# Kernel optimization log

Measured on AMD Instinct MI355X. Metric: run time of the kernel, lower is better.

Reference implementation:

```python
import jax, jax.numpy as jnp
import numpy as np

DIM = 768
NH = 12
HD = DIM // NH
HIDDEN = 4 * DIM
Z_SIZE = (8, 8)
X_SIZE = (16, 16)
SCALE = HD ** -0.5
LN_EPS = 1e-5


def _rel_index(q_size, kv_size):
    hq, wq = q_size
    hk, wk = kv_size
    cq = np.stack(np.meshgrid(np.arange(hq), np.arange(wq), indexing='ij'), -1).reshape(-1, 2)
    ck = np.stack(np.meshgrid(np.arange(hk), np.arange(wk), indexing='ij'), -1).reshape(-1, 2)
    rel = cq[:, None, :] - ck[None, :, :]  # (Lq, Lk, 2)
    rel[..., 0] += hk - 1
    rel[..., 1] += wk - 1
    return jnp.asarray(rel[..., 0] * (wq + wk - 1) + rel[..., 1])  # (Lq, Lk)

ZX_IDX = _rel_index(Z_SIZE, X_SIZE)  # (64, 256)
XZ_IDX = _rel_index(X_SIZE, Z_SIZE)  # (256, 64)


def _ln(v, g, b):
    m = jnp.mean(v, -1, keepdims=True)
    var = jnp.var(v, -1, keepdims=True)
    return (v - m) * jax.lax.rsqrt(var + LN_EPS) * g + b


def _cross_attn(q_in, kv_in, qw, qb, kvw, kvb, pw, pb, rpb, idx):
    B, Lq, D = q_in.shape
    Lk = kv_in.shape[1]
    q = (q_in @ qw.T + qb).reshape(B, Lq, NH, HD).transpose(0, 2, 1, 3)  # (B,H,Lq,hd)
    kv = (kv_in @ kvw.T + kvb).reshape(B, Lk, 2, NH, HD).transpose(2, 0, 3, 1, 4)
    k, v = kv[0], kv[1]  # (B,H,Lk,hd)
    bias = rpb[idx].transpose(2, 0, 1)  # (H,Lq,Lk)
    attn = jnp.einsum('bhqd,bhkd->bhqk', q, k) * SCALE + bias[None]
    attn = jax.nn.softmax(attn, axis=-1)
    o = jnp.einsum('bhqk,bhkd->bhqd', attn, v).transpose(0, 2, 1, 3).reshape(B, Lq, D)
    return o @ pw.T + pb


def _mlp(v, w1, b1, w2, b2):
    return jax.nn.gelu(v @ w1.T + b1, approximate=False) @ w2.T + b2


def setup_inputs() -> dict:
    key = jax.random.key(0)
    ks = jax.random.split(key, 24)
    w = lambda k, s: jax.random.normal(k, s, jnp.float32) * 0.02
    TBL = (Z_SIZE[0] + X_SIZE[0] - 1) * (Z_SIZE[1] + X_SIZE[1] - 1)  # 529
    return {
        'z': jax.random.normal(ks[0], (64, 64, DIM), jnp.float32),
        'x': jax.random.normal(ks[1], (64, 256, DIM), jnp.float32),
        'z_ln1_g': jnp.ones((DIM,), jnp.float32), 'z_ln1_b': jnp.zeros((DIM,), jnp.float32),
        'x_ln1_g': jnp.ones((DIM,), jnp.float32), 'x_ln1_b': jnp.zeros((DIM,), jnp.float32),
        'zx_qw': w(ks[2], (DIM, DIM)), 'zx_qb': jnp.zeros((DIM,), jnp.float32),
        'zx_kvw': w(ks[3], (2 * DIM, DIM)), 'zx_kvb': jnp.zeros((2 * DIM,), jnp.float32),
        'zx_pw': w(ks[4], (DIM, DIM)), 'zx_pb': jnp.zeros((DIM,), jnp.float32),
        'zx_rpb': w(ks[5], (TBL, NH)),
        'xz_qw': w(ks[6], (DIM, DIM)), 'xz_qb': jnp.zeros((DIM,), jnp.float32),
        'xz_kvw': w(ks[7], (2 * DIM, DIM)), 'xz_kvb': jnp.zeros((2 * DIM,), jnp.float32),
        'xz_pw': w(ks[8], (DIM, DIM)), 'xz_pb': jnp.zeros((DIM,), jnp.float32),
        'xz_rpb': w(ks[9], (TBL, NH)),
        'z_ln2_g': jnp.ones((DIM,), jnp.float32), 'z_ln2_b': jnp.zeros((DIM,), jnp.float32),
        'z_fc1_w': w(ks[10], (HIDDEN, DIM)), 'z_fc1_b': jnp.zeros((HIDDEN,), jnp.float32),
        'z_fc2_w': w(ks[11], (DIM, HIDDEN)), 'z_fc2_b': jnp.zeros((DIM,), jnp.float32),
        'x_ln2_g': jnp.ones((DIM,), jnp.float32), 'x_ln2_b': jnp.zeros((DIM,), jnp.float32),
        'x_fc1_w': w(ks[12], (HIDDEN, DIM)), 'x_fc1_b': jnp.zeros((HIDDEN,), jnp.float32),
        'x_fc2_w': w(ks[13], (DIM, HIDDEN)), 'x_fc2_b': jnp.zeros((DIM,), jnp.float32),
    }


def reference(z, x, z_ln1_g, z_ln1_b, x_ln1_g, x_ln1_b,
              zx_qw, zx_qb, zx_kvw, zx_kvb, zx_pw, zx_pb, zx_rpb,
              xz_qw, xz_qb, xz_kvw, xz_kvb, xz_pw, xz_pb, xz_rpb,
              z_ln2_g, z_ln2_b, z_fc1_w, z_fc1_b, z_fc2_w, z_fc2_b,
              x_ln2_g, x_ln2_b, x_fc1_w, x_fc1_b, x_fc2_w, x_fc2_b):
    zn = _ln(z, z_ln1_g, z_ln1_b)
    xn = _ln(x, x_ln1_g, x_ln1_b)
    z_attn = _cross_attn(zn, xn, zx_qw, zx_qb, zx_kvw, zx_kvb, zx_pw, zx_pb, zx_rpb, ZX_IDX)
    x_attn = _cross_attn(xn, zn, xz_qw, xz_qb, xz_kvw, xz_kvb, xz_pw, xz_pb, xz_rpb, XZ_IDX)
    z2 = z + z_attn
    z2 = z2 + _mlp(_ln(z2, z_ln2_g, z_ln2_b), z_fc1_w, z_fc1_b, z_fc2_w, z_fc2_b)
    x2 = x + x_attn
    x2 = x2 + _mlp(_ln(x2, x_ln2_g, x_ln2_b), x_fc1_w, x_fc1_b, x_fc2_w, x_fc2_b)
    return (z2, x2)
```

## Files before the change

### kernel.cpp

```cpp
#include <hip/hip_runtime.h>
#include <math.h>

typedef unsigned short u16;
typedef unsigned int u32;
typedef __attribute__((ext_vector_type(8))) short bf16x8;
typedef __attribute__((ext_vector_type(4))) float f32x4;
typedef __attribute__((ext_vector_type(4))) u16 u16x4;

__device__ __forceinline__ u16 f2bf(float f) {
  u32 u = __builtin_bit_cast(u32, f);
  u32 r = (u + 0x7fffu + ((u >> 16) & 1u)) >> 16;
  return (u16)r;
}

__device__ __forceinline__ float gelu_f(float v) {
  float u = 1.5957691216057308f * v * (1.0f + 0.044715f * v * v);
  return v / (1.0f + __expf(-u));
}

__device__ __forceinline__ void async16(const void* g, void* l) {
  __builtin_amdgcn_global_load_lds(
      (__attribute__((address_space(1))) void*)(unsigned long long)(const char*)g,
      (__attribute__((address_space(3))) void*)l, 16, 0, 0);
}

#define SCHED0 __builtin_amdgcn_sched_barrier(0)
#define BARRIER __builtin_amdgcn_s_barrier()

__device__ __forceinline__ void ln_rows4(
    const float* __restrict__ in1, const float* __restrict__ g1, const float* __restrict__ b1,
    u16* __restrict__ out1, int rows1,
    const float* __restrict__ in2, const float* __restrict__ g2v, const float* __restrict__ b2v,
    u16* __restrict__ out2, int rowblk)
{
  const int w = threadIdx.x >> 6;
  const int lane = threadIdx.x & 63;
  const int row = rowblk * 4 + w;
  const float* in; const float* gg; const float* bb; u16* out;
  if (row < rows1) { in = in1 + (size_t)row * 768; gg = g1; bb = b1; out = out1 + (size_t)row * 768; }
  else { const int r2 = row - rows1; in = in2 + (size_t)r2 * 768; gg = g2v; bb = b2v; out = out2 + (size_t)r2 * 768; }

  float4 v0 = *(const float4*)&in[lane * 4];
  float4 v1 = *(const float4*)&in[lane * 4 + 256];
  float4 v2 = *(const float4*)&in[lane * 4 + 512];
  float s = v0.x + v0.y + v0.z + v0.w + v1.x + v1.y + v1.z + v1.w + v2.x + v2.y + v2.z + v2.w;
  float s2 = v0.x*v0.x + v0.y*v0.y + v0.z*v0.z + v0.w*v0.w
           + v1.x*v1.x + v1.y*v1.y + v1.z*v1.z + v1.w*v1.w
           + v2.x*v2.x + v2.y*v2.y + v2.z*v2.z + v2.w*v2.w;
#pragma unroll
  for (int m = 1; m <= 32; m <<= 1) { s += __shfl_xor(s, m); s2 += __shfl_xor(s2, m); }
  const float mean = s * (1.0f / 768.0f);
  const float var = s2 * (1.0f / 768.0f) - mean * mean;
  const float rs = rsqrtf(var + 1e-5f);

#define LNSTORE(V, OFFS) { \
    float4 gv = *(const float4*)&gg[lane * 4 + OFFS]; \
    float4 bv = *(const float4*)&bb[lane * 4 + OFFS]; \
    u16x4 o; \
    o.x = f2bf((V.x - mean) * rs * gv.x + bv.x); \
    o.y = f2bf((V.y - mean) * rs * gv.y + bv.y); \
    o.z = f2bf((V.z - mean) * rs * gv.z + bv.z); \
    o.w = f2bf((V.w - mean) * rs * gv.w + bv.w); \
    *(u16x4*)&out[lane * 4 + OFFS] = o; }
  LNSTORE(v0, 0)
  LNSTORE(v1, 256)
  LNSTORE(v2, 512)
#undef LNSTORE
}

__global__ __launch_bounds__(256) void ln_dual(
    const float* __restrict__ in1, const float* __restrict__ g1, const float* __restrict__ b1,
    u16* __restrict__ out1, int rows1,
    const float* __restrict__ in2, const float* __restrict__ g2, const float* __restrict__ b2,
    u16* __restrict__ out2)
{
  ln_rows4(in1, g1, b1, out1, rows1, in2, g2, b2, out2, blockIdx.x);
}

struct PrepArgs {
  const float* csrc[10]; u16* cdst[10]; int cn[10];
  const float* z; const float* zg; const float* zb; u16* zo;
  const float* x; const float* xg; const float* xb; u16* xo;
  const float* zq; const float* zkv; const float* xq; const float* xkv;
  float* bz; float* bx;
};

__global__ __launch_bounds__(256) void prep(PrepArgs a) {
  const int b = blockIdx.x;
  if (b < 23040) {
    const int seg = b / 2304;
    const long i = ((long)(b % 2304) * 256 + threadIdx.x) * 4;
    if (i >= a.cn[seg]) return;
    float4 v = *(const float4*)&a.csrc[seg][i];
    u16x4 o;
    o.x = f2bf(v.x); o.y = f2bf(v.y); o.z = f2bf(v.z); o.w = f2bf(v.w);
    *(u16x4*)&a.cdst[seg][i] = o;
  } else if (b < 28160) {
    ln_rows4(a.z, a.zg, a.zb, a.zo, 4096, a.x, a.xg, a.xb, a.xo, b - 23040);
  } else {
    const int i = (b - 28160) * 256 + threadIdx.x;
    if (i >= 2304) return;
    a.bz[i] = (i < 768) ? a.zq[i] : a.zkv[i - 768];
    a.bx[i] = (i < 768) ? a.xq[i] : a.xkv[i - 768];
  }
}

template<int EPI>
__device__ __forceinline__ void gemm6_core(
    const u16* __restrict__ A, const u16* __restrict__ W,
    const float* __restrict__ bias, const float* __restrict__ res,
    void* __restrict__ outp, long row0, long col0, int N, int K)
{
  __shared__ __align__(16) u16 As[3][256 * 32];
  __shared__ __align__(16) u16 Bs[3][128 * 32];

  const int tid = threadIdx.x;
  const int lane = tid & 63;
  const int w = tid >> 6;
  const int wm = w >> 1;
  const int wn = w & 1;

  const u16* gA[2];
  const u16* gB;
#pragma unroll
  for (int l = 0; l < 2; ++l) {
    const int e = l * 512 + tid;
    const int r = e >> 2, sl = e & 3;
    gA[l] = A + (row0 + r) * (long)K + ((sl ^ ((r >> 1) & 3)) * 8);
  }
  {
    const int r = tid >> 2, sl = tid & 3;
    gB = W + (col0 + r) * (long)K + ((sl ^ ((r >> 1) & 3)) * 8);
  }

  const int fr = lane & 15;
  const int g = lane >> 4;

  f32x4 acc[4][4];
#pragma unroll
  for (int m = 0; m < 4; ++m)
#pragma unroll
    for (int n = 0; n < 4; ++n) acc[m][n] = (f32x4){0.f, 0.f, 0.f, 0.f};

  auto stage = [&](u16* ab, u16* bb, long ko) {
#pragma unroll
    for (int l = 0; l < 2; ++l) async16(gA[l] + ko, &ab[(l * 512 + tid) * 8]);
    async16(gB + ko, &bb[tid * 8]);
  };

  const int nt = K / 32;
  u16 *a0 = &As[0][0], *a1 = &As[1][0], *a2 = &As[2][0];
  u16 *b0 = &Bs[0][0], *b1 = &Bs[1][0], *b2 = &Bs[2][0];

  stage(a0, b0, 0);
  stage(a1, b1, 32);
  SCHED0;
  asm volatile("s_waitcnt vmcnt(3)" ::: "memory");
  BARRIER;
  SCHED0;

  for (int t = 0; t < nt; ++t) {
    if (t + 2 < nt) stage(a2, b2, (long)(t + 2) * 32);
    SCHED0;
    bf16x8 bfr[4];
#pragma unroll
    for (int n = 0; n < 4; ++n) {
      const int r = wn * 64 + n * 16 + fr;
      bfr[n] = *(const bf16x8*)&b0[r * 32 + ((g ^ ((r >> 1) & 3)) * 8)];
    }
    __builtin_amdgcn_s_setprio(1);
#pragma unroll
    for (int m = 0; m < 4; ++m) {
      const int r = wm * 64 + m * 16 + fr;
      bf16x8 af = *(const bf16x8*)&a0[r * 32 + ((g ^ ((r >> 1) & 3)) * 8)];
#pragma unroll
      for (int n = 0; n < 4; ++n)
        acc[m][n] = __builtin_amdgcn_mfma_f32_16x16x32_bf16(af, bfr[n], acc[m][n], 0, 0, 0);
    }
    __builtin_amdgcn_s_setprio(0);
    SCHED0;
    if (t + 2 < nt) {
      asm volatile("s_waitcnt vmcnt(3) lgkmcnt(0)" ::: "memory");
    } else if (t + 1 < nt) {
      asm volatile("s_waitcnt vmcnt(0) lgkmcnt(0)" ::: "memory");
    }
    if (t + 1 < nt) { BARRIER; SCHED0; }
    u16* ta = a0; a0 = a1; a1 = a2; a2 = ta;
    u16* tb = b0; b0 = b1; b1 = b2; b2 = tb;
  }

  float bv[4];
#pragma unroll
  for (int n = 0; n < 4; ++n) bv[n] = bias[col0 + wn * 64 + n * 16 + fr];
#pragma unroll
  for (int m = 0; m < 4; ++m) {
#pragma unroll
    for (int j = 0; j < 4; ++j) {
      const long row = row0 + wm * 64 + m * 16 + g * 4 + j;
      const long base = row * N + col0 + wn * 64 + fr;
#pragma unroll
      for (int n = 0; n < 4; ++n) {
        float v = acc[m][n][j] + bv[n];
        if constexpr (EPI == 0) {
          ((u16*)outp)[base + n * 16] = f2bf(v);
        } else if constexpr (EPI == 1) {
          ((u16*)outp)[base + n * 16] = f2bf(gelu_f(v));
        } else {
          ((float*)outp)[base + n * 16] = v + res[base + n * 16];
        }
      }
    }
  }
}

template<int EPI>
__global__ __launch_bounds__(512, 4) void gemm6(
    const u16* __restrict__ A, const u16* __restrict__ W,
    const float* __restrict__ bias, const float* __restrict__ res,
    void* __restrict__ outp, int M, int N, int K)
{
  int flat = blockIdx.y * gridDim.x + blockIdx.x;
  const int nwg = gridDim.x * gridDim.y;
  if ((nwg & 7) == 0) flat = (flat & 7) * (nwg >> 3) + (flat >> 3);
  const int bx = flat % gridDim.x;
  const int by = flat / gridDim.x;
  gemm6_core<EPI>(A, W, bias, res, outp, (long)by * 256, (long)bx * 128, N, K);
}

template<int EPI>
__global__ __launch_bounds__(512, 4) void gemm6f(
    const u16* __restrict__ A0, const u16* __restrict__ W0,
    const float* __restrict__ bias0, const float* __restrict__ res0, void* __restrict__ out0,
    const u16* __restrict__ A1, const u16* __restrict__ W1,
    const float* __restrict__ bias1, const float* __restrict__ res1, void* __restrict__ out1,
    int Y0, int N, int K)
{
  int flat = blockIdx.y * gridDim.x + blockIdx.x;
  const int nwg = gridDim.x * gridDim.y;
  if ((nwg & 7) == 0) flat = (flat & 7) * (nwg >> 3) + (flat >> 3);
  const int bx = flat % gridDim.x;
  const int by = flat / gridDim.x;
  if (by < Y0) {
    gemm6_core<EPI>(A0, W0, bias0, res0, out0, (long)by * 256, (long)bx * 128, N, K);
  } else {
    gemm6_core<EPI>(A1, W1, bias1, res1, out1, (long)(by - Y0) * 256, (long)bx * 128, N, K);
  }
}

template<int LQ>
__device__ __forceinline__ int rel_index(int q, int k) {
  if constexpr (LQ == 64) {
    const int qh = q >> 3, qw = q & 7, kh = k >> 4, kw = k & 15;
    return (qh - kh + 15) * 23 + (qw - kw + 15);
  } else {
    const int qh = q >> 4, qw = q & 15, kh = k >> 3, kw = k & 7;
    return (qh - kh + 7) * 23 + (qw - kw + 7);
  }
}

template<int LQ, int LK>
__device__ void attn_core(
    const u16* __restrict__ Q, int qs, const u16* __restrict__ KV, int ks,
    const float* __restrict__ rpb, u16* __restrict__ O, char* sm, int h, int b)
{
  constexpr int MT = LQ / 64;
  constexpr int NT = LK / 16;
  constexpr int KSPV = LK / 32;

  u16* Qs = (u16*)sm;
  u16* Ks = Qs + LQ * 64;
  u16* Vt = Ks + LK * 64;
  u16* Ps = Vt + 64 * LK;
  float* bias_s = (float*)(Ps + (size_t)LQ * LK);

  const int tid = threadIdx.x;
  const int lane = tid & 63;
  const int w = tid >> 6;

  for (int i = tid; i < 529; i += 256) bias_s[i] = rpb[i * 12 + h];

#pragma unroll
  for (int it = 0; it < LQ * 8 / 256; ++it) {
    const int s = it * 256 + tid;
    const int r = s >> 3, sl2 = s & 7;
    bf16x8 v = *(const bf16x8*)&Q[(size_t)(b * LQ + r) * qs + h * 64 + sl2 * 8];
    *(bf16x8*)&Qs[r * 64 + ((sl2 ^ (r & 7)) * 8)] = v;
  }
#pragma unroll
  for (int it = 0; it < LK * 8 / 256; ++it) {
    const int s = it * 256 + tid;
    const int r = s >> 3, sl2 = s & 7;
    bf16x8 v = *(const bf16x8*)&KV[(size_t)(b * LK + r) * ks + h * 64 + sl2 * 8];
    *(bf16x8*)&Ks[r * 64 + ((sl2 ^ (r & 7)) * 8)] = v;
  }
#pragma unroll
  for (int it = 0; it < LK * 8 / 256; ++it) {
    const int s = it * 256 + tid;
    const int r = s >> 3, sl2 = s & 7;
    const int d0 = sl2 * 8;
    bf16x8 v = *(const bf16x8*)&KV[(size_t)(b * LK + r) * ks + 768 + h * 64 + d0];
#pragma unroll
    for (int j = 0; j < 8; ++j) {
      const int d = d0 + j;
      Vt[d * LK + (((r >> 3) ^ (d & 7)) * 8) + (r & 7)] = (u16)v[j];
    }
  }
  __syncthreads();

  const int fr = lane & 15;
  const int g = lane >> 4;
  const int qbase = w * MT * 16;

  f32x4 sacc[MT][NT];
#pragma unroll
  for (int mt = 0; mt < MT; ++mt)
#pragma unroll
    for (int nt = 0; nt < NT; ++nt) sacc[mt][nt] = (f32x4){0.f, 0.f, 0.f, 0.f};

#pragma unroll
  for (int mt = 0; mt < MT; ++mt) {
    const int qr = qbase + mt * 16 + fr;
    bf16x8 aq0 = *(const bf16x8*)&Qs[qr * 64 + (((0 + g) ^ (qr & 7)) * 8)];
    bf16x8 aq1 = *(const bf16x8*)&Qs[qr * 64 + (((4 + g) ^ (qr & 7)) * 8)];
#pragma unroll
    for (int nt = 0; nt < NT; ++nt) {
      const int kr = nt * 16 + fr;
      bf16x8 bk0 = *(const bf16x8*)&Ks[kr * 64 + (((0 + g) ^ (kr & 7)) * 8)];
      bf16x8 bk1 = *(const bf16x8*)&Ks[kr * 64 + (((4 + g) ^ (kr & 7)) * 8)];
      sacc[mt][nt] = __builtin_amdgcn_mfma_f32_16x16x32_bf16(aq0, bk0, sacc[mt][nt], 0, 0, 0);
      sacc[mt][nt] = __builtin_amdgcn_mfma_f32_16x16x32_bf16(aq1, bk1, sacc[mt][nt], 0, 0, 0);
    }
  }

#pragma unroll
  for (int mt = 0; mt < MT; ++mt) {
#pragma unroll
    for (int reg = 0; reg < 4; ++reg) {
      const int q = qbase + mt * 16 + g * 4 + reg;
      float mx = -3.0e38f;
#pragma unroll
      for (int nt = 0; nt < NT; ++nt) {
        const int k = nt * 16 + fr;
        float s = sacc[mt][nt][reg] * 0.125f + bias_s[rel_index<LQ>(q, k)];
        sacc[mt][nt][reg] = s;
        mx = fmaxf(mx, s);
      }
      mx = fmaxf(mx, __shfl_xor(mx, 1));
      mx = fmaxf(mx, __shfl_xor(mx, 2));
      mx = fmaxf(mx, __shfl_xor(mx, 4));
      mx = fmaxf(mx, __shfl_xor(mx, 8));
      float sum = 0.f;
#pragma unroll
      for (int nt = 0; nt < NT; ++nt) {
        float p = __expf(sacc[mt][nt][reg] - mx);
        sacc[mt][nt][reg] = p;
        sum += p;
      }
      sum += __shfl_xor(sum, 1);
      sum += __shfl_xor(sum, 2);
      sum += __shfl_xor(sum, 4);
      sum += __shfl_xor(sum, 8);
      const float inv = 1.0f / sum;
#pragma unroll
      for (int nt = 0; nt < NT; ++nt) {
        const int k = nt * 16 + fr;
        Ps[q * LK + (((k >> 3) ^ (q & 7)) * 8) + (k & 7)] = f2bf(sacc[mt][nt][reg] * inv);
      }
    }
  }
  __syncthreads();

  f32x4 oacc[MT][4];
#pragma unroll
  for (int mt = 0; mt < MT; ++mt)
#pragma unroll
    for (int n = 0; n < 4; ++n) oacc[mt][n] = (f32x4){0.f, 0.f, 0.f, 0.f};

#pragma unroll
  for (int mt = 0; mt < MT; ++mt) {
    const int pr = qbase + mt * 16 + fr;
#pragma unroll
    for (int ks2 = 0; ks2 < KSPV; ++ks2) {
      bf16x8 ap = *(const bf16x8*)&Ps[pr * LK + (((ks2 * 4 + g) ^ (pr & 7)) * 8)];
#pragma unroll
      for (int n = 0; n < 4; ++n) {
        const int d = n * 16 + fr;
        bf16x8 bvv = *(const bf16x8*)&Vt[d * LK + (((ks2 * 4 + g) ^ (d & 7)) * 8)];
        oacc[mt][n] = __builtin_amdgcn_mfma_f32_16x16x32_bf16(ap, bvv, oacc[mt][n], 0, 0, 0);
      }
    }
  }

#pragma unroll
  for (int mt = 0; mt < MT; ++mt)
#pragma unroll
    for (int n = 0; n < 4; ++n)
#pragma unroll
      for (int reg = 0; reg < 4; ++reg) {
        const int q = qbase + mt * 16 + g * 4 + reg;
        const int d = n * 16 + fr;
        O[(size_t)(b * LQ + q) * 768 + h * 64 + d] = f2bf(oacc[mt][n][reg]);
      }
}

__global__ __launch_bounds__(256) void attn_both(
    const u16* __restrict__ qkv_z, const u16* __restrict__ qkv_x,
    const float* __restrict__ zx_rpb, const float* __restrict__ xz_rpb,
    u16* __restrict__ ao_z, u16* __restrict__ ao_x)
{
  __shared__ __align__(16) char sm[108624];
  const int h = blockIdx.x, b = blockIdx.y;
  if (blockIdx.z == 0)
    attn_core<64, 256>(qkv_z, 2304, qkv_x + 768, 2304, zx_rpb, ao_z, sm, h, b);
  else
    attn_core<256, 64>(qkv_x, 2304, qkv_z + 768, 2304, xz_rpb, ao_x, sm, h, b);
}

extern "C" void kernel_launch(void* const* d_in, const int* in_sizes, int n_in,
                              void* d_out, int out_size, void* d_ws, size_t ws_size,
                              hipStream_t stream)
{
  const float* z      = (const float*)d_in[0];
  const float* x      = (const float*)d_in[1];
  const float* zln1g  = (const float*)d_in[2];
  const float* zln1b  = (const float*)d_in[3];
  const float* xln1g  = (const float*)d_in[4];
  const float* xln1b  = (const float*)d_in[5];
  const float* zx_qw  = (const float*)d_in[6];
  const float* zx_qb  = (const float*)d_in[7];
  const float* zx_kvw = (const float*)d_in[8];
  const float* zx_kvb = (const float*)d_in[9];
  const float* zx_pw  = (const float*)d_in[10];
  const float* zx_pb  = (const float*)d_in[11];
  const float* zx_rpb = (const float*)d_in[12];
  const float* xz_qw  = (const float*)d_in[13];
  const float* xz_qb  = (const float*)d_in[14];
  const float* xz_kvw = (const float*)d_in[15];
  const float* xz_kvb = (const float*)d_in[16];
  const float* xz_pw  = (const float*)d_in[17];
  const float* xz_pb  = (const float*)d_in[18];
  const float* xz_rpb = (const float*)d_in[19];
  const float* zln2g  = (const float*)d_in[20];
  const float* zln2b  = (const float*)d_in[21];
  const float* zfc1w  = (const float*)d_in[22];
  const float* zfc1b  = (const float*)d_in[23];
  const float* zfc2w  = (const float*)d_in[24];
  const float* zfc2b  = (const float*)d_in[25];
  const float* xln2g  = (const float*)d_in[26];
  const float* xln2b  = (const float*)d_in[27];
  const float* xfc1w  = (const float*)d_in[28];
  const float* xfc1b  = (const float*)d_in[29];
  const float* xfc2w  = (const float*)d_in[30];
  const float* xfc2b  = (const float*)d_in[31];

  float* out = (float*)d_out;
  float* z2 = out;
  float* x2 = out + 3145728;

  char* ws = (char*)d_ws;
  size_t off = 0;
  auto take = [&](size_t bytes) {
    char* p = ws + off;
    off += (bytes + 255) & ~(size_t)255;
    return p;
  };
  u16* w_zn   = (u16*)take(1769472 * 2);
  u16* w_xn   = (u16*)take(1769472 * 2);
  u16* w_zx_p = (u16*)take(589824 * 2);
  u16* w_xz_p = (u16*)take(589824 * 2);
  u16* w_zfc1 = (u16*)take(2359296 * 2);
  u16* w_zfc2 = (u16*)take(2359296 * 2);
  u16* w_xfc1 = (u16*)take(2359296 * 2);
  u16* w_xfc2 = (u16*)take(2359296 * 2);
  float* b_zn = (float*)take(2304 * 4);
  float* b_xn = (float*)take(2304 * 4);
  u16* regA   = (u16*)take(31457280);

  const size_t need_full = off + 125829120;
  const bool full = (ws_size >= need_full);
  u16* regB = (u16*)take(full ? 125829120 : 94371840);

  u16* zn    = regA;
  u16* xn    = regA + 3145728;
  u16* qkv_z = regB;
  u16* qkv_x = regB + 9437184;
  u16* ao_z  = zn;
  u16* ao_x  = xn;
  u16* z2n   = zn;
  u16* x2n   = xn;
  u16* hz    = regB;
  u16* hx    = regB + 12582912;

  PrepArgs a;
  a.csrc[0] = zx_qw;  a.cdst[0] = w_zn;           a.cn[0] = 589824;
  a.csrc[1] = xz_kvw; a.cdst[1] = w_zn + 589824;  a.cn[1] = 1179648;
  a.csrc[2] = xz_qw;  a.cdst[2] = w_xn;           a.cn[2] = 589824;
  a.csrc[3] = zx_kvw; a.cdst[3] = w_xn + 589824;  a.cn[3] = 1179648;
  a.csrc[4] = zx_pw;  a.cdst[4] = w_zx_p;         a.cn[4] = 589824;
  a.csrc[5] = xz_pw;  a.cdst[5] = w_xz_p;         a.cn[5] = 589824;
  a.csrc[6] = zfc1w;  a.cdst[6] = w_zfc1;         a.cn[6] = 2359296;
  a.csrc[7] = zfc2w;  a.cdst[7] = w_zfc2;         a.cn[7] = 2359296;
  a.csrc[8] = xfc1w;  a.cdst[8] = w_xfc1;         a.cn[8] = 2359296;
  a.csrc[9] = xfc2w;  a.cdst[9] = w_xfc2;         a.cn[9] = 2359296;
  a.z = z; a.zg = zln1g; a.zb = zln1b; a.zo = zn;
  a.x = x; a.xg = xln1g; a.xb = xln1b; a.xo = xn;
  a.zq = zx_qb; a.zkv = xz_kvb; a.xq = xz_qb; a.xkv = zx_kvb;
  a.bz = b_zn; a.bx = b_xn;
  prep<<<28169, 256, 0, stream>>>(a);

  gemm6f<0><<<dim3(18, 80), 512, 0, stream>>>(
      zn, w_zn, b_zn, nullptr, qkv_z,
      xn, w_xn, b_xn, nullptr, qkv_x, 16, 2304, 768);

  attn_both<<<dim3(12, 64, 2), 256, 0, stream>>>(qkv_z, qkv_x, zx_rpb, xz_rpb, ao_z, ao_x);

  gemm6f<2><<<dim3(6, 80), 512, 0, stream>>>(
      ao_z, w_zx_p, zx_pb, z, z2,
      ao_x, w_xz_p, xz_pb, x, x2, 16, 768, 768);

  ln_dual<<<5120, 256, 0, stream>>>(z2, zln2g, zln2b, z2n, 4096, x2, xln2g, xln2b, x2n);

  if (full) {
    gemm6f<1><<<dim3(24, 80), 512, 0, stream>>>(
        z2n, w_zfc1, zfc1b, nullptr, hz,
        x2n, w_xfc1, xfc1b, nullptr, hx, 16, 3072, 768);
    gemm6f<2><<<dim3(6, 80), 512, 0, stream>>>(
        hz, w_zfc2, zfc2b, z2, z2,
        hx, w_xfc2, xfc2b, x2, x2, 16, 768, 3072);
  } else {
    gemm6f<1><<<dim3(24, 48), 512, 0, stream>>>(
        z2n, w_zfc1, zfc1b, nullptr, hz,
        x2n, w_xfc1, xfc1b, nullptr, hx, 16, 3072, 768);
    gemm6f<2><<<dim3(6, 48), 512, 0, stream>>>(
        hz, w_zfc2, zfc2b, z2, z2,
        hx, w_xfc2, xfc2b, x2, x2, 16, 768, 3072);
    gemm6<1><<<dim3(24, 32), 512, 0, stream>>>(x2n + (size_t)8192 * 768, w_xfc1, xfc1b, nullptr, hx, 8192, 3072, 768);
    gemm6<2><<<dim3(6, 32),  512, 0, stream>>>(hx, w_xfc2, xfc2b, x2 + (size_t)8192 * 768, x2 + (size_t)8192 * 768, 8192, 768, 3072);
  }
}
```

Baseline: 511.6 us.

## Load GEMM weight fragments directly from global memory instead of staging through LDS

After: 825.5 us. 1.61x slower.

```diff
diff --git a/kernel.cpp b/kernel.cpp
--- a/kernel.cpp
+++ b/kernel.cpp
@@ -106,13 +106,12 @@
 }
 
 template<int EPI>
-__device__ __forceinline__ void gemm6_core(
+__device__ __forceinline__ void gemm7_core(
     const u16* __restrict__ A, const u16* __restrict__ W,
     const float* __restrict__ bias, const float* __restrict__ res,
     void* __restrict__ outp, long row0, long col0, int N, int K)
 {
   __shared__ __align__(16) u16 As[3][256 * 32];
-  __shared__ __align__(16) u16 Bs[3][128 * 32];
 
   const int tid = threadIdx.x;
   const int lane = tid & 63;
@@ -121,72 +120,74 @@
   const int wn = w & 1;
 
   const u16* gA[2];
-  const u16* gB;
 #pragma unroll
   for (int l = 0; l < 2; ++l) {
     const int e = l * 512 + tid;
     const int r = e >> 2, sl = e & 3;
     gA[l] = A + (row0 + r) * (long)K + ((sl ^ ((r >> 1) & 3)) * 8);
   }
-  {
-    const int r = tid >> 2, sl = tid & 3;
-    gB = W + (col0 + r) * (long)K + ((sl ^ ((r >> 1) & 3)) * 8);
-  }
 
   const int fr = lane & 15;
   const int g = lane >> 4;
 
+  const u16* gW[4];
+#pragma unroll
+  for (int n = 0; n < 4; ++n)
+    gW[n] = W + (col0 + wn * 64 + n * 16 + fr) * (long)K + g * 8;
+
   f32x4 acc[4][4];
 #pragma unroll
   for (int m = 0; m < 4; ++m)
 #pragma unroll
     for (int n = 0; n < 4; ++n) acc[m][n] = (f32x4){0.f, 0.f, 0.f, 0.f};
-
-  auto stage = [&](u16* ab, u16* bb, long ko) {
-#pragma unroll
-    for (int l = 0; l < 2; ++l) async16(gA[l] + ko, &ab[(l * 512 + tid) * 8]);
-    async16(gB + ko, &bb[tid * 8]);
-  };
 
   const int nt = K / 32;
   u16 *a0 = &As[0][0], *a1 = &As[1][0], *a2 = &As[2][0];
-  u16 *b0 = &Bs[0][0], *b1 = &Bs[1][0], *b2 = &Bs[2][0];
-
-  stage(a0, b0, 0);
-  stage(a1, b1, 32);
+
+  async16(gA[0], &a0[(0 * 512 + tid) * 8]);
+  async16(gA[1], &a0[(1 * 512 + tid) * 8]);
+  async16(gA[0] + 32, &a1[(0 * 512 + tid) * 8]);
+  async16(gA[1] + 32, &a1[(1 * 512 + tid) * 8]);
   SCHED0;
-  asm volatile("s_waitcnt vmcnt(3)" ::: "memory");
+  asm volatile("s_waitcnt vmcnt(2)" ::: "memory");
   BARRIER;
   SCHED0;
 
   for (int t = 0; t < nt; ++t) {
-    if (t + 2 < nt) stage(a2, b2, (long)(t + 2) * 32);
+    const long ko = (long)t * 32;
+    bf16x8 bfr[4];
+#pragma unroll
+    for (int n = 0; n < 4; ++n) bfr[n] = *(const bf16x8*)(gW[n] + ko);
     SCHED0;
-    bf16x8 bfr[4];
-#pragma unroll
-    for (int n = 0; n < 4; ++n) {
-      const int r = wn * 64 + n * 16 + fr;
-      bfr[n] = *(const bf16x8*)&b0[r * 32 + ((g ^ ((r >> 1) & 3)) * 8)];
-    }
-    __builtin_amdgcn_s_setprio(1);
+    if (t + 2 < nt) {
+      const long ks = ko + 64;
+      async16(gA[0] + ks, &a2[(0 * 512 + tid) * 8]);
+      async16(gA[1] + ks, &a2[(1 * 512 + tid) * 8]);
+    }
+    SCHED0;
+    bf16x8 af[4];
 #pragma unroll
     for (int m = 0; m < 4; ++m) {
       const int r = wm * 64 + m * 16 + fr;
-      bf16x8 af = *(const bf16x8*)&a0[r * 32 + ((g ^ ((r >> 1) & 3)) * 8)];
+      af[m] = *(const bf16x8*)&a0[r * 32 + ((g ^ ((r >> 1) & 3)) * 8)];
+    }
+    SCHED0;
+    if (t + 2 < nt) {
+      asm volatile("s_waitcnt vmcnt(2) lgkmcnt(0)" ::: "memory");
+    } else {
+      asm volatile("s_waitcnt vmcnt(0) lgkmcnt(0)" ::: "memory");
+    }
+    SCHED0;
+    __builtin_amdgcn_s_setprio(1);
+#pragma unroll
+    for (int m = 0; m < 4; ++m)
 #pragma unroll
       for (int n = 0; n < 4; ++n)
-        acc[m][n] = __builtin_amdgcn_mfma_f32_16x16x32_bf16(af, bfr[n], acc[m][n], 0, 0, 0);
-    }
+        acc[m][n] = __builtin_amdgcn_mfma_f32_16x16x32_bf16(af[m], bfr[n], acc[m][n], 0, 0, 0);
     __builtin_amdgcn_s_setprio(0);
     SCHED0;
-    if (t + 2 < nt) {
-      asm volatile("s_waitcnt vmcnt(3) lgkmcnt(0)" ::: "memory");
-    } else if (t + 1 < nt) {
-      asm volatile("s_waitcnt vmcnt(0) lgkmcnt(0)" ::: "memory");
-    }
     if (t + 1 < nt) { BARRIER; SCHED0; }
     u16* ta = a0; a0 = a1; a1 = a2; a2 = ta;
-    u16* tb = b0; b0 = b1; b1 = b2; b2 = tb;
   }
 
   float bv[4];
@@ -214,7 +215,7 @@
 }
 
 template<int EPI>
-__global__ __launch_bounds__(512, 4) void gemm6(
+__global__ __launch_bounds__(512, 4) void gemm7(
     const u16* __restrict__ A, const u16* __restrict__ W,
     const float* __restrict__ bias, const float* __restrict__ res,
     void* __restrict__ outp, int M, int N, int K)
@@ -224,11 +225,11 @@
   if ((nwg & 7) == 0) flat = (flat & 7) * (nwg >> 3) + (flat >> 3);
   const int bx = flat % gridDim.x;
   const int by = flat / gridDim.x;
-  gemm6_core<EPI>(A, W, bias, res, outp, (long)by * 256, (long)bx * 128, N, K);
+  gemm7_core<EPI>(A, W, bias, res, outp, (long)by * 256, (long)bx * 128, N, K);
 }
 
 template<int EPI>
-__global__ __launch_bounds__(512, 4) void gemm6f(
+__global__ __launch_bounds__(512, 4) void gemm7f(
     const u16* __restrict__ A0, const u16* __restrict__ W0,
     const float* __restrict__ bias0, const float* __restrict__ res0, void* __restrict__ out0,
     const u16* __restrict__ A1, const u16* __restrict__ W1,
@@ -241,9 +242,9 @@
   const int bx = flat % gridDim.x;
   const int by = flat / gridDim.x;
   if (by < Y0) {
-    gemm6_core<EPI>(A0, W0, bias0, res0, out0, (long)by * 256, (long)bx * 128, N, K);
+    gemm7_core<EPI>(A0, W0, bias0, res0, out0, (long)by * 256, (long)bx * 128, N, K);
   } else {
-    gemm6_core<EPI>(A1, W1, bias1, res1, out1, (long)(by - Y0) * 256, (long)bx * 128, N, K);
+    gemm7_core<EPI>(A1, W1, bias1, res1, out1, (long)(by - Y0) * 256, (long)bx * 128, N, K);
   }
 }
 
@@ -508,33 +509,33 @@
   a.bz = b_zn; a.bx = b_xn;
   prep<<<28169, 256, 0, stream>>>(a);
 
-  gemm6f<0><<<dim3(18, 80), 512, 0, stream>>>(
+  gemm7f<0><<<dim3(18, 80), 512, 0, stream>>>(
       zn, w_zn, b_zn, nullptr, qkv_z,
       xn, w_xn, b_xn, nullptr, qkv_x, 16, 2304, 768);
 
   attn_both<<<dim3(12, 64, 2), 256, 0, stream>>>(qkv_z, qkv_x, zx_rpb, xz_rpb, ao_z, ao_x);
 
-  gemm6f<2><<<dim3(6, 80), 512, 0, stream>>>(
+  gemm7f<2><<<dim3(6, 80), 512, 0, stream>>>(
       ao_z, w_zx_p, zx_pb, z, z2,
       ao_x, w_xz_p, xz_pb, x, x2, 16, 768, 768);
 
   ln_dual<<<5120, 256, 0, stream>>>(z2, zln2g, zln2b, z2n, 4096, x2, xln2g, xln2b, x2n);
 
   if (full) {
-    gemm6f<1><<<dim3(24, 80), 512, 0, stream>>>(
+    gemm7f<1><<<dim3(24, 80), 512, 0, stream>>>(
         z2n, w_zfc1, zfc1b, nullptr, hz,
         x2n, w_xfc1, xfc1b, nullptr, hx, 16, 3072, 768);
-    gemm6f<2><<<dim3(6, 80), 512, 0, stream>>>(
+    gemm7f<2><<<dim3(6, 80), 512, 0, stream>>>(
         hz, w_zfc2, zfc2b, z2, z2,
         hx, w_xfc2, xfc2b, x2, x2, 16, 768, 3072);
   } else {
-    gemm6f<1><<<dim3(24, 48), 512, 0, stream>>>(
+    gemm7f<1><<<dim3(24, 48), 512, 0, stream>>>(
         z2n, w_zfc1, zfc1b, nullptr, hz,
         x2n, w_xfc1, xfc1b, nullptr, hx, 16, 3072, 768);
-    gemm6f<2><<<dim3(6, 48), 512, 0, stream>>>(
+    gemm7f<2><<<dim3(6, 48), 512, 0, stream>>>(
         hz, w_zfc2, zfc2b, z2, z2,
         hx, w_xfc2, xfc2b, x2, x2, 16, 768, 3072);
-    gemm6<1><<<dim3(24, 32), 512, 0, stream>>>(x2n + (size_t)8192 * 768, w_xfc1, xfc1b, nullptr, hx, 8192, 3072, 768);
-    gemm6<2><<<dim3(6, 32),  512, 0, stream>>>(hx, w_xfc2, xfc2b, x2 + (size_t)8192 * 768, x2 + (size_t)8192 * 768, 8192, 768, 3072);
-  }
-}
+    gemm7<1><<<dim3(24, 32), 512, 0, stream>>>(x2n + (size_t)8192 * 768, w_xfc1, xfc1b, nullptr, hx, 8192, 3072, 768);
+    gemm7<2><<<dim3(6, 32),  512, 0, stream>>>(hx, w_xfc2, xfc2b, x2 + (size_t)8192 * 768, x2 + (size_t)8192 * 768, 8192, 768, 3072);
+  }
+}
```

## Switch GEMMs to 128x128 tiles with 256 threads and double buffering

Applied to the files above, without the earlier changes.

After: 549.6 us. 1.07x slower.

```diff
diff --git a/kernel.cpp b/kernel.cpp
--- a/kernel.cpp
+++ b/kernel.cpp
@@ -25,7 +25,6 @@
 }
 
 #define SCHED0 __builtin_amdgcn_sched_barrier(0)
-#define BARRIER __builtin_amdgcn_s_barrier()
 
 __device__ __forceinline__ void ln_rows4(
     const float* __restrict__ in1, const float* __restrict__ g1, const float* __restrict__ b1,
@@ -106,13 +105,13 @@
 }
 
 template<int EPI>
-__device__ __forceinline__ void gemm6_core(
+__device__ __forceinline__ void gemm9u_core(
     const u16* __restrict__ A, const u16* __restrict__ W,
     const float* __restrict__ bias, const float* __restrict__ res,
     void* __restrict__ outp, long row0, long col0, int N, int K)
 {
-  __shared__ __align__(16) u16 As[3][256 * 32];
-  __shared__ __align__(16) u16 Bs[3][128 * 32];
+  __shared__ __align__(16) u16 As[2][128 * 32];
+  __shared__ __align__(16) u16 Bs[2][128 * 32];
 
   const int tid = threadIdx.x;
   const int lane = tid & 63;
@@ -120,74 +119,81 @@
   const int wm = w >> 1;
   const int wn = w & 1;
 
-  const u16* gA[2];
-  const u16* gB;
-#pragma unroll
-  for (int l = 0; l < 2; ++l) {
-    const int e = l * 512 + tid;
-    const int r = e >> 2, sl = e & 3;
-    gA[l] = A + (row0 + r) * (long)K + ((sl ^ ((r >> 1) & 3)) * 8);
-  }
+  const u16* gA0; const u16* gA1; const u16* gB0; const u16* gB1;
   {
-    const int r = tid >> 2, sl = tid & 3;
-    gB = W + (col0 + r) * (long)K + ((sl ^ ((r >> 1) & 3)) * 8);
-  }
+    const int e0 = tid, e1 = 256 + tid;
+    const int r0 = e0 >> 2, s0 = (e0 & 3) ^ ((r0 >> 1) & 3);
+    const int r1 = e1 >> 2, s1 = (e1 & 3) ^ ((r1 >> 1) & 3);
+    gA0 = A + (row0 + r0) * (long)K + s0 * 8;
+    gA1 = A + (row0 + r1) * (long)K + s1 * 8;
+    gB0 = W + (col0 + r0) * (long)K + s0 * 8;
+    gB1 = W + (col0 + r1) * (long)K + s1 * 8;
+  }
+  const int sd0 = tid * 8, sd1 = (256 + tid) * 8;
 
   const int fr = lane & 15;
   const int g = lane >> 4;
 
+  int aoff[4], boff[4];
+#pragma unroll
+  for (int m = 0; m < 4; ++m) {
+    const int r = wm * 64 + m * 16 + fr;
+    aoff[m] = r * 32 + ((g ^ ((r >> 1) & 3)) * 8);
+  }
+#pragma unroll
+  for (int n = 0; n < 4; ++n) {
+    const int r = wn * 64 + n * 16 + fr;
+    boff[n] = r * 32 + ((g ^ ((r >> 1) & 3)) * 8);
+  }
+
   f32x4 acc[4][4];
 #pragma unroll
   for (int m = 0; m < 4; ++m)
 #pragma unroll
     for (int n = 0; n < 4; ++n) acc[m][n] = (f32x4){0.f, 0.f, 0.f, 0.f};
 
-  auto stage = [&](u16* ab, u16* bb, long ko) {
-#pragma unroll
-    for (int l = 0; l < 2; ++l) async16(gA[l] + ko, &ab[(l * 512 + tid) * 8]);
-    async16(gB + ko, &bb[tid * 8]);
-  };
-
   const int nt = K / 32;
-  u16 *a0 = &As[0][0], *a1 = &As[1][0], *a2 = &As[2][0];
-  u16 *b0 = &Bs[0][0], *b1 = &Bs[1][0], *b2 = &Bs[2][0];
-
-  stage(a0, b0, 0);
-  stage(a1, b1, 32);
-  SCHED0;
-  asm volatile("s_waitcnt vmcnt(3)" ::: "memory");
-  BARRIER;
-  SCHED0;
-
-  for (int t = 0; t < nt; ++t) {
-    if (t + 2 < nt) stage(a2, b2, (long)(t + 2) * 32);
-    SCHED0;
-    bf16x8 bfr[4];
-#pragma unroll
-    for (int n = 0; n < 4; ++n) {
-      const int r = wn * 64 + n * 16 + fr;
-      bfr[n] = *(const bf16x8*)&b0[r * 32 + ((g ^ ((r >> 1) & 3)) * 8)];
-    }
-    __builtin_amdgcn_s_setprio(1);
-#pragma unroll
-    for (int m = 0; m < 4; ++m) {
-      const int r = wm * 64 + m * 16 + fr;
-      bf16x8 af = *(const bf16x8*)&a0[r * 32 + ((g ^ ((r >> 1) & 3)) * 8)];
-#pragma unroll
-      for (int n = 0; n < 4; ++n)
-        acc[m][n] = __builtin_amdgcn_mfma_f32_16x16x32_bf16(af, bfr[n], acc[m][n], 0, 0, 0);
-    }
-    __builtin_amdgcn_s_setprio(0);
-    SCHED0;
-    if (t + 2 < nt) {
-      asm volatile("s_waitcnt vmcnt(3) lgkmcnt(0)" ::: "memory");
-    } else if (t + 1 < nt) {
-      asm volatile("s_waitcnt vmcnt(0) lgkmcnt(0)" ::: "memory");
-    }
-    if (t + 1 < nt) { BARRIER; SCHED0; }
-    u16* ta = a0; a0 = a1; a1 = a2; a2 = ta;
-    u16* tb = b0; b0 = b1; b1 = b2; b2 = tb;
-  }
+  int ko = 32;
+
+  async16(gA0, &As[0][sd0]);
+  async16(gA1, &As[0][sd1]);
+  async16(gB0, &Bs[0][sd0]);
+  async16(gB1, &Bs[0][sd1]);
+  __syncthreads();
+
+#define G9_STEP(BUF, DOSTAGE)                                                 \
+  {                                                                           \
+    if (DOSTAGE) {                                                            \
+      async16(gA0 + ko, &As[BUF ^ 1][sd0]);                                   \
+      async16(gA1 + ko, &As[BUF ^ 1][sd1]);                                   \
+      async16(gB0 + ko, &Bs[BUF ^ 1][sd0]);                                   \
+      async16(gB1 + ko, &Bs[BUF ^ 1][sd1]);                                   \
+      ko += 32;                                                               \
+    }                                                                         \
+    SCHED0;                                                                   \
+    bf16x8 bfr[4], af[4];                                                     \
+    _Pragma("unroll")                                                         \
+    for (int n = 0; n < 4; ++n) bfr[n] = *(const bf16x8*)&Bs[BUF][boff[n]];   \
+    _Pragma("unroll")                                                         \
+    for (int m = 0; m < 4; ++m) af[m] = *(const bf16x8*)&As[BUF][aoff[m]];    \
+    __builtin_amdgcn_s_setprio(1);                                            \
+    _Pragma("unroll")                                                         \
+    for (int m = 0; m < 4; ++m)                                               \
+      _Pragma("unroll")                                                       \
+      for (int n = 0; n < 4; ++n)                                             \
+        acc[m][n] = __builtin_amdgcn_mfma_f32_16x16x32_bf16(af[m], bfr[n],    \
+                                                            acc[m][n], 0,0,0);\
+    __builtin_amdgcn_s_setprio(0);                                            \
+    __syncthreads();                                                          \
+  }
+
+  for (int t = 0; t < nt - 2; t += 2) {
+    G9_STEP(0, true)
+    G9_STEP(1, true)
+  }
+  G9_STEP(0, true)
+  G9_STEP(1, false)
+#undef G9_STEP
 
   float bv[4];
 #pragma unroll
@@ -214,7 +220,7 @@
 }
 
 template<int EPI>
-__global__ __launch_bounds__(512, 4) void gemm6(
+__global__ __launch_bounds__(256, 4) void gemm9u(
     const u16* __restrict__ A, const u16* __restrict__ W,
     const float* __restrict__ bias, const float* __restrict__ res,
     void* __restrict__ outp, int M, int N, int K)
@@ -224,11 +230,11 @@
   if ((nwg & 7) == 0) flat = (flat & 7) * (nwg >> 3) + (flat >> 3);
   const int bx = flat % gridDim.x;
   const int by = flat / gridDim.x;
-  gemm6_core<EPI>(A, W, bias, res, outp, (long)by * 256, (long)bx * 128, N, K);
+  gemm9u_core<EPI>(A, W, bias, res, outp, (long)by * 128, (long)bx * 128, N, K);
 }
 
 template<int EPI>
-__global__ __launch_bounds__(512, 4) void gemm6f(
+__global__ __launch_bounds__(256, 4) void gemm9uf(
     const u16* __restrict__ A0, const u16* __restrict__ W0,
     const float* __restrict__ bias0, const float* __restrict__ res0, void* __restrict__ out0,
     const u16* __restrict__ A1, const u16* __restrict__ W1,
@@ -241,9 +247,9 @@
   const int bx = flat % gridDim.x;
   const int by = flat / gridDim.x;
   if (by < Y0) {
-    gemm6_core<EPI>(A0, W0, bias0, res0, out0, (long)by * 256, (long)bx * 128, N, K);
+    gemm9u_core<EPI>(A0, W0, bias0, res0, out0, (long)by * 128, (long)bx * 128, N, K);
   } else {
-    gemm6_core<EPI>(A1, W1, bias1, res1, out1, (long)(by - Y0) * 256, (long)bx * 128, N, K);
+    gemm9u_core<EPI>(A1, W1, bias1, res1, out1, (long)(by - Y0) * 128, (long)bx * 128, N, K);
   }
 }
 
@@ -508,33 +514,33 @@
   a.bz = b_zn; a.bx = b_xn;
   prep<<<28169, 256, 0, stream>>>(a);
 
-  gemm6f<0><<<dim3(18, 80), 512, 0, stream>>>(
+  gemm9uf<0><<<dim3(18, 160), 256, 0, stream>>>(
       zn, w_zn, b_zn, nullptr, qkv_z,
-      xn, w_xn, b_xn, nullptr, qkv_x, 16, 2304, 768);
+      xn, w_xn, b_xn, nullptr, qkv_x, 32, 2304, 768);
 
   attn_both<<<dim3(12, 64, 2), 256, 0, stream>>>(qkv_z, qkv_x, zx_rpb, xz_rpb, ao_z, ao_x);
 
-  gemm6f<2><<<dim3(6, 80), 512, 0, stream>>>(
+  gemm9uf<2><<<dim3(6, 160), 256, 0, stream>>>(
       ao_z, w_zx_p, zx_pb, z, z2,
-      ao_x, w_xz_p, xz_pb, x, x2, 16, 768, 768);
+      ao_x, w_xz_p, xz_pb, x, x2, 32, 768, 768);
 
   ln_dual<<<5120, 256, 0, stream>>>(z2, zln2g, zln2b, z2n, 4096, x2, xln2g, xln2b, x2n);
 
   if (full) {
-    gemm6f<1><<<dim3(24, 80), 512, 0, stream>>>(
+    gemm9uf<1><<<dim3(24, 160), 256, 0, stream>>>(
         z2n, w_zfc1, zfc1b, nullptr, hz,
-        x2n, w_xfc1, xfc1b, nullptr, hx, 16, 3072, 768);
-    gemm6f<2><<<dim3(6, 80), 512, 0, stream>>>(
+        x2n, w_xfc1, xfc1b, nullptr, hx, 32, 3072, 768);
+    gemm9uf<2><<<dim3(6, 160), 256, 0, stream>>>(
         hz, w_zfc2, zfc2b, z2, z2,
-        hx, w_xfc2, xfc2b, x2, x2, 16, 768, 3072);
+        hx, w_xfc2, xfc2b, x2, x2, 32, 768, 3072);
   } else {
-    gemm6f<1><<<dim3(24, 48), 512, 0, stream>>>(
+    gemm9uf<1><<<dim3(24, 96), 256, 0, stream>>>(
         z2n, w_zfc1, zfc1b, nullptr, hz,
-        x2n, w_xfc1, xfc1b, nullptr, hx, 16, 3072, 768);
-    gemm6f<2><<<dim3(6, 48), 512, 0, stream>>>(
+        x2n, w_xfc1, xfc1b, nullptr, hx, 32, 3072, 768);
+    gemm9uf<2><<<dim3(6, 96), 256, 0, stream>>>(
         hz, w_zfc2, zfc2b, z2, z2,
-        hx, w_xfc2, xfc2b, x2, x2, 16, 768, 3072);
-    gemm6<1><<<dim3(24, 32), 512, 0, stream>>>(x2n + (size_t)8192 * 768, w_xfc1, xfc1b, nullptr, hx, 8192, 3072, 768);
-    gemm6<2><<<dim3(6, 32),  512, 0, stream>>>(hx, w_xfc2, xfc2b, x2 + (size_t)8192 * 768, x2 + (size_t)8192 * 768, 8192, 768, 3072);
-  }
-}
+        hx, w_xfc2, xfc2b, x2, x2, 32, 768, 3072);
+    gemm9u<1><<<dim3(24, 64), 256, 0, stream>>>(x2n + (size_t)8192 * 768, w_xfc1, xfc1b, nullptr, hx, 8192, 3072, 768);
+    gemm9u<2><<<dim3(6, 64), 256, 0, stream>>>(hx, w_xfc2, xfc2b, x2 + (size_t)8192 * 768, x2 + (size_t)8192 * 768, 8192, 768, 3072);
+  }
+}
```
